# Performance work log

Hardware: AMD Instinct MI355X
Metric: run time of the kernel (lower is better)

The kernel has to match this reference:

```python
import jax, jax.numpy as jnp
import numpy as np

EPS = 1e-6

def _rms_norm(t, g):
    # t: [B, S, C] (applied before the view to heads, matching the torch code)
    y = t.astype(jnp.float32)
    y = jax.lax.rsqrt(jnp.mean(y * y, axis=-1, keepdims=True) + EPS)
    return (t * y * g).astype(t.dtype)

def _apply_rope(t, cos, sin):
    # t: [B, S, N, D]; cos/sin: [1, S, 1, D//2]; interleaved pair rotation
    b, s, n, d = t.shape
    tr = t.reshape(b, s, n, d // 2, 2)
    tre, tim = tr[..., 0], tr[..., 1]
    out = jnp.stack([tre * cos - tim * sin, tre * sin + tim * cos], axis=-1)
    return out.reshape(b, s, n, d)

def setup_inputs() -> dict:
    key = jax.random.key(0)
    ks = jax.random.split(key, 8)
    B, S, DIM, N, D = 2, 1024, 3072, 24, 128
    x = jax.random.normal(ks[0], (B, S, DIM), dtype=jnp.float32)
    seq_lens = jax.random.randint(ks[1], (B,), S // 2, S + 1, dtype=jnp.int32)
    grid_sizes = jnp.tile(jnp.array([[16, 8, 8]], dtype=jnp.int32), (B, 1))
    # rope angle table [1024, D//2]: pos * inv_freq
    inv_freq = 1.0 / (10000.0 ** (jnp.arange(D // 2, dtype=jnp.float32) * 2.0 / D))
    freqs = jnp.arange(1024, dtype=jnp.float32)[:, None] * inv_freq[None, :]
    sc = 1.0 / np.sqrt(DIM)
    Wq = jax.random.normal(ks[2], (DIM, DIM), dtype=jnp.float32) * sc
    Wk = jax.random.normal(ks[3], (DIM, DIM), dtype=jnp.float32) * sc
    Wv = jax.random.normal(ks[4], (DIM, DIM), dtype=jnp.float32) * sc
    Wo = jax.random.normal(ks[5], (DIM, DIM), dtype=jnp.float32) * sc
    bq = jnp.zeros((DIM,), jnp.float32); bk = jnp.zeros((DIM,), jnp.float32)
    bv = jnp.zeros((DIM,), jnp.float32); bo = jnp.zeros((DIM,), jnp.float32)
    gq = jnp.ones((DIM,), jnp.float32); gk = jnp.ones((DIM,), jnp.float32)
    return {"x": x, "seq_lens": seq_lens, "grid_sizes": grid_sizes, "freqs": freqs,
            "Wq": Wq, "bq": bq, "Wk": Wk, "bk": bk, "Wv": Wv, "bv": bv,
            "Wo": Wo, "bo": bo, "gq": gq, "gk": gk}

def reference(x, seq_lens, grid_sizes, freqs, Wq, bq, Wk, bk, Wv, bv, Wo, bo, gq, gk):
    b, s, dim = x.shape
    d = 2 * freqs.shape[1]          # head_dim
    n = dim // d                    # num_heads
    q = _rms_norm(x @ Wq.T + bq, gq).reshape(b, s, n, d)
    k = _rms_norm(x @ Wk.T + bk, gk).reshape(b, s, n, d)
    v = (x @ Wv.T + bv).reshape(b, s, n, d)
    ang = freqs[:s]                 # [S, D//2]
    cos = jnp.cos(ang)[None, :, None, :]
    sin = jnp.sin(ang)[None, :, None, :]
    q = _apply_rope(q, cos, sin)
    k = _apply_rope(k, cos, sin)
    # full attention (window_size = (-1,-1)), varlen key masking via seq_lens
    scale = d ** -0.5
    scores = jnp.einsum('bind,bjnd->bnij', q, k) * scale   # [B,N,S,S]
    key_valid = jnp.arange(s)[None, :] < seq_lens[:, None]  # [B,S]
    scores = jnp.where(key_valid[:, None, None, :], scores, jnp.finfo(scores.dtype).min)
    p = jax.nn.softmax(scores, axis=-1)
    out = jnp.einsum('bnij,bjnd->bind', p, v).reshape(b, s, dim)
    return out @ Wo.T + bo
```

## Files before the change

### kernel.cpp

```cpp
#include <hip/hip_runtime.h>
#include <cmath>

#define BB   2
#define SS   1024
#define DIMM 3072
#define NHH  24
#define HDD  128
#define MM   (BB * SS)

typedef _Float16 f16;
typedef __attribute__((ext_vector_type(8))) _Float16 half8;
typedef __attribute__((ext_vector_type(4))) float floatx4;
typedef unsigned int u32;
typedef const __attribute__((address_space(1))) u32* gp1;
typedef __attribute__((address_space(3))) u32* lp3;

__device__ __forceinline__ void gload_lds16(const void* g, void* l) {
    __builtin_amdgcn_global_load_lds((gp1)g, (lp3)l, 16, 0, 0);
}

__global__ __launch_bounds__(256) void cvt_f16_kernel(
    const float* __restrict__ in, f16* __restrict__ outp, int n8)
{
    int i = blockIdx.x * 256 + threadIdx.x;
    if (i >= n8) return;
    const float4* p = (const float4*)(in + (size_t)i * 8);
    float4 a = p[0], b = p[1];
    half8 h = {(f16)a.x, (f16)a.y, (f16)a.z, (f16)a.w,
               (f16)b.x, (f16)b.y, (f16)b.z, (f16)b.w};
    *(half8*)(outp + (size_t)i * 8) = h;
}

__global__ __launch_bounds__(256) void cvt3_f16_kernel(
    const float* __restrict__ w0, const float* __restrict__ w1,
    const float* __restrict__ w2, f16* __restrict__ outp, int n8each)
{
    int i = blockIdx.x * 256 + threadIdx.x;
    int sel = i / n8each;
    int j = i - sel * n8each;
    const float* in = sel == 0 ? w0 : (sel == 1 ? w1 : w2);
    const float4* p = (const float4*)(in + (size_t)j * 8);
    float4 a = p[0], b = p[1];
    half8 h = {(f16)a.x, (f16)a.y, (f16)a.z, (f16)a.w,
               (f16)b.x, (f16)b.y, (f16)b.z, (f16)b.w};
    *(half8*)(outp + (size_t)i * 8) = h;
}

__global__ __launch_bounds__(256) void cvt4_f16_kernel(
    const float* __restrict__ w0, const float* __restrict__ w1,
    const float* __restrict__ w2, const float* __restrict__ w3,
    f16* __restrict__ outp, int n8each)
{
    int i = blockIdx.x * 256 + threadIdx.x;
    int sel = i / n8each;
    int j = i - sel * n8each;
    const float* in = sel == 0 ? w0 : (sel == 1 ? w1 : (sel == 2 ? w2 : w3));
    const float4* p = (const float4*)(in + (size_t)j * 8);
    float4 a = p[0], b = p[1];
    half8 h = {(f16)a.x, (f16)a.y, (f16)a.z, (f16)a.w,
               (f16)b.x, (f16)b.y, (f16)b.z, (f16)b.w};
    *(half8*)(outp + (size_t)i * 8) = h;
}

template<bool QKV>
__global__ __launch_bounds__(256) void gemm_p32d4(
    const f16* __restrict__ A,
    const f16* __restrict__ W0, const f16* __restrict__ W1, const f16* __restrict__ W2,
    const float* __restrict__ b0, const float* __restrict__ b1, const float* __restrict__ b2,
    f16* __restrict__ D0, f16* __restrict__ D1, f16* __restrict__ D2,
    float* __restrict__ F)
{
    constexpr int K = DIMM;
    constexpr int NSTEP = K / 32;
    constexpr int TS = 128 * 32;
    __shared__ __align__(16) f16 As[5][TS];
    __shared__ __align__(16) f16 Bs[5][TS];

    const int tid  = threadIdx.x;
    const int lane = tid & 63;
    const int wave = tid >> 6;
    const int wm = wave >> 1, wn = wave & 1;
    const int lr = lane & 15;
    const int lq = lane >> 4;

    const int id  = blockIdx.x;
    const int cpx = (int)gridDim.x >> 3;
    const int swz = (id & 7) * cpx + (id >> 3);
    const int bm = (swz & 15) << 7;
    const int bn = (swz >> 4) << 7;

    const f16* Wh; const float* bias; f16* D = nullptr;
    int nloc = bn;
    if constexpr (QKV) {
        int sel = bn / DIMM;
        nloc = bn - sel * DIMM;
        Wh   = sel == 0 ? W0 : (sel == 1 ? W1 : W2);
        bias = sel == 0 ? b0 : (sel == 1 ? b1 : b2);
        D    = sel == 0 ? D0 : (sel == 1 ? D1 : D2);
    } else { Wh = W0; bias = b0; }

    const int r0 = tid >> 2;
    const int g0 = ((tid & 3) ^ ((r0 >> 1) & 3)) << 3;
    const int r1 = (tid + 256) >> 2;
    const int g1 = ((tid & 3) ^ ((r1 >> 1) & 3)) << 3;
    const f16* a0  = A  + (size_t)(bm   + r0) * K + g0;
    const f16* a1  = A  + (size_t)(bm   + r1) * K + g1;
    const f16* w0p = Wh + (size_t)(nloc + r0) * K + g0;
    const f16* w1p = Wh + (size_t)(nloc + r1) * K + g1;

    auto STAGE = [&](int t, int buf) {
        const int k0 = t * 32;
        gload_lds16(a0  + k0, &As[buf][(size_t)tid * 8]);
        gload_lds16(a1  + k0, &As[buf][(size_t)(tid + 256) * 8]);
        gload_lds16(w0p + k0, &Bs[buf][(size_t)tid * 8]);
        gload_lds16(w1p + k0, &Bs[buf][(size_t)(tid + 256) * 8]);
    };

    floatx4 acc[4][4];
#pragma unroll
    for (int i = 0; i < 4; ++i)
#pragma unroll
        for (int j = 0; j < 4; ++j) acc[i][j] = (floatx4){0.f, 0.f, 0.f, 0.f};

    auto COMPUTE = [&](int buf) {
        const f16* Ab = &As[buf][0];
        const f16* Bb = &Bs[buf][0];
        half8 af[4], bf[4];
#pragma unroll
        for (int i = 0; i < 4; ++i) {
            int ra = wm * 64 + i * 16 + lr;
            int rb = wn * 64 + i * 16 + lr;
            af[i] = *(const half8*)&Ab[ra * 32 + ((lq ^ ((ra >> 1) & 3)) << 3)];
            bf[i] = *(const half8*)&Bb[rb * 32 + ((lq ^ ((rb >> 1) & 3)) << 3)];
        }
#pragma unroll
        for (int mi = 0; mi < 4; ++mi)
#pragma unroll
            for (int ni = 0; ni < 4; ++ni)
                acc[mi][ni] = __builtin_amdgcn_mfma_f32_16x16x32_f16(af[mi], bf[ni], acc[mi][ni], 0, 0, 0);
    };

    STAGE(0, 0); STAGE(1, 1); STAGE(2, 2); STAGE(3, 3);
    asm volatile("s_waitcnt vmcnt(12)" ::: "memory");
    __builtin_amdgcn_s_barrier();

    int cur = 0, stg = 4;
    for (int ks = 0; ks < NSTEP; ++ks) {
        if (ks + 4 < NSTEP) STAGE(ks + 4, stg);
        COMPUTE(cur);
        const int rem = NSTEP - ks;
        if (rem > 4)       asm volatile("s_waitcnt vmcnt(12)" ::: "memory");
        else if (rem == 4) asm volatile("s_waitcnt vmcnt(8)"  ::: "memory");
        else if (rem == 3) asm volatile("s_waitcnt vmcnt(4)"  ::: "memory");
        else if (rem == 2) asm volatile("s_waitcnt vmcnt(0)"  ::: "memory");
        if (rem > 1) __builtin_amdgcn_s_barrier();
        cur = (cur == 4) ? 0 : cur + 1;
        stg = (stg == 4) ? 0 : stg + 1;
    }

    const int crow0 = bm + wm * 64 + (lq << 2);
    const int ccol0 = nloc + wn * 64;
#pragma unroll
    for (int ni = 0; ni < 4; ++ni) {
        const int col = ccol0 + ni * 16 + lr;
        const float bv = bias[col];
#pragma unroll
        for (int mi = 0; mi < 4; ++mi) {
            const int row = crow0 + mi * 16;
#pragma unroll
            for (int r2 = 0; r2 < 4; ++r2) {
                if constexpr (QKV)
                    D[(size_t)(row + r2) * DIMM + col] = (f16)(acc[mi][ni][r2] + bv);
                else
                    F[(size_t)(row + r2) * DIMM + col] = acc[mi][ni][r2] + bv;
            }
        }
    }
}

template<bool QKV>
__global__ __launch_bounds__(256) void gemm_p32(
    const f16* __restrict__ A,
    const f16* __restrict__ W0, const f16* __restrict__ W1, const f16* __restrict__ W2,
    const float* __restrict__ b0, const float* __restrict__ b1, const float* __restrict__ b2,
    f16* __restrict__ D0, f16* __restrict__ D1, f16* __restrict__ D2,
    float* __restrict__ F)
{
    constexpr int K = DIMM;
    constexpr int NSTEP = K / 32;
    constexpr int TS = 128 * 32;
    __shared__ __align__(16) f16 As[3][TS];
    __shared__ __align__(16) f16 Bs[3][TS];

    const int tid  = threadIdx.x;
    const int lane = tid & 63;
    const int wave = tid >> 6;
    const int wm = wave >> 1, wn = wave & 1;
    const int lr = lane & 15;
    const int lq = lane >> 4;

    const int id  = blockIdx.x;
    const int cpx = (int)gridDim.x >> 3;
    const int swz = (id & 7) * cpx + (id >> 3);
    const int bm = (swz & 15) << 7;
    const int bn = (swz >> 4) << 7;

    const f16* Wh; const float* bias; f16* D = nullptr;
    int nloc = bn;
    if constexpr (QKV) {
        int sel = bn / DIMM;
        nloc = bn - sel * DIMM;
        Wh   = sel == 0 ? W0 : (sel == 1 ? W1 : W2);
        bias = sel == 0 ? b0 : (sel == 1 ? b1 : b2);
        D    = sel == 0 ? D0 : (sel == 1 ? D1 : D2);
    } else { Wh = W0; bias = b0; }

    const int r0 = tid >> 2;
    const int g0 = ((tid & 3) ^ ((r0 >> 1) & 3)) << 3;
    const int r1 = (tid + 256) >> 2;
    const int g1 = ((tid & 3) ^ ((r1 >> 1) & 3)) << 3;
    const f16* a0  = A  + (size_t)(bm   + r0) * K + g0;
    const f16* a1  = A  + (size_t)(bm   + r1) * K + g1;
    const f16* w0p = Wh + (size_t)(nloc + r0) * K + g0;
    const f16* w1p = Wh + (size_t)(nloc + r1) * K + g1;

    auto STAGE = [&](int t, int buf) {
        const int k0 = t * 32;
        gload_lds16(a0  + k0, &As[buf][(size_t)tid * 8]);
        gload_lds16(a1  + k0, &As[buf][(size_t)(tid + 256) * 8]);
        gload_lds16(w0p + k0, &Bs[buf][(size_t)tid * 8]);
        gload_lds16(w1p + k0, &Bs[buf][(size_t)(tid + 256) * 8]);
    };

    floatx4 acc[4][4];
#pragma unroll
    for (int i = 0; i < 4; ++i)
#pragma unroll
        for (int j = 0; j < 4; ++j) acc[i][j] = (floatx4){0.f, 0.f, 0.f, 0.f};

    auto COMPUTE = [&](int buf) {
        const f16* Ab = &As[buf][0];
        const f16* Bb = &Bs[buf][0];
        half8 af[4], bf[4];
#pragma unroll
        for (int i = 0; i < 4; ++i) {
            int ra = wm * 64 + i * 16 + lr;
            int rb = wn * 64 + i * 16 + lr;
            af[i] = *(const half8*)&Ab[ra * 32 + ((lq ^ ((ra >> 1) & 3)) << 3)];
            bf[i] = *(const half8*)&Bb[rb * 32 + ((lq ^ ((rb >> 1) & 3)) << 3)];
        }
#pragma unroll
        for (int mi = 0; mi < 4; ++mi)
#pragma unroll
            for (int ni = 0; ni < 4; ++ni)
                acc[mi][ni] = __builtin_amdgcn_mfma_f32_16x16x32_f16(af[mi], bf[ni], acc[mi][ni], 0, 0, 0);
    };

    STAGE(0, 0);
    STAGE(1, 1);
    asm volatile("s_waitcnt vmcnt(4)" ::: "memory");
    __builtin_amdgcn_s_barrier();

    int cur = 0, stg = 2;
    for (int ks = 0; ks < NSTEP; ++ks) {
        const bool more = (ks + 2 < NSTEP);
        if (more) STAGE(ks + 2, stg);
        COMPUTE(cur);
        if (more) asm volatile("s_waitcnt vmcnt(4)" ::: "memory");
        else      asm volatile("s_waitcnt vmcnt(0)" ::: "memory");
        __builtin_amdgcn_s_barrier();
        cur = (cur == 2) ? 0 : cur + 1;
        stg = (stg == 2) ? 0 : stg + 1;
    }

    const int crow0 = bm + wm * 64 + (lq << 2);
    const int ccol0 = nloc + wn * 64;
#pragma unroll
    for (int ni = 0; ni < 4; ++ni) {
        const int col = ccol0 + ni * 16 + lr;
        const float bv = bias[col];
#pragma unroll
        for (int mi = 0; mi < 4; ++mi) {
            const int row = crow0 + mi * 16;
#pragma unroll
            for (int r2 = 0; r2 < 4; ++r2) {
                if constexpr (QKV)
                    D[(size_t)(row + r2) * DIMM + col] = (f16)(acc[mi][ni][r2] + bv);
                else
                    F[(size_t)(row + r2) * DIMM + col] = acc[mi][ni][r2] + bv;
            }
        }
    }
}

template<bool QKV>
__global__ __launch_bounds__(256) void gemm_f16m(
    const f16* __restrict__ A,
    const float* __restrict__ W0, const float* __restrict__ W1, const float* __restrict__ W2,
    const float* __restrict__ b0, const float* __restrict__ b1, const float* __restrict__ b2,
    f16* __restrict__ D0, f16* __restrict__ D1, f16* __restrict__ D2,
    float* __restrict__ F)
{
    constexpr int K = DIMM;
    constexpr int NSTEP = K / 32;
    __shared__ f16 As[128 * 32];
    __shared__ f16 Bs[128 * 32];

    const int tid  = threadIdx.x;
    const int lane = tid & 63;
    const int wave = tid >> 6;
    const int wm = wave >> 1, wn = wave & 1;
    const int lr = lane & 15;
    const int lq = lane >> 4;

    const int id  = blockIdx.x;
    const int cpx = (int)gridDim.x >> 3;
    const int swz = (id & 7) * cpx + (id >> 3);
    const int bm = (swz & 15) << 7;
    const int bn = (swz >> 4) << 7;

    const float* W; const float* bias; f16* D = nullptr;
    int nloc = bn;
    if constexpr (QKV) {
        int sel = bn / DIMM;
        nloc = bn - sel * DIMM;
        W    = sel == 0 ? W0 : (sel == 1 ? W1 : W2);
        bias = sel == 0 ? b0 : (sel == 1 ? b1 : b2);
        D    = sel == 0 ? D0 : (sel == 1 ? D1 : D2);
    } else { W = W0; bias = b0; }

    const int r0 = tid >> 2;
    const int c8 = (tid & 3) << 3;
    const float* bp0 = W + (size_t)(nloc + r0) * K + c8;
    const float* bp1 = W + (size_t)(nloc + r0 + 64) * K + c8;

    const int arow_l = lane >> 2;
    const int acol_l = (lane & 3) << 3;
    const f16* agbase = A + (size_t)bm * K;

    float4 sb00, sb01, sb10, sb11;
    auto LOADB = [&](int k0) {
        sb00 = *(const float4*)(bp0 + k0); sb01 = *(const float4*)(bp0 + k0 + 4);
        sb10 = *(const float4*)(bp1 + k0); sb11 = *(const float4*)(bp1 + k0 + 4);
    };
    auto STOREB = [&]() {
        half8 h0 = {(f16)sb00.x, (f16)sb00.y, (f16)sb00.z, (f16)sb00.w,
                    (f16)sb01.x, (f16)sb01.y, (f16)sb01.z, (f16)sb01.w};
        half8 h1 = {(f16)sb10.x, (f16)sb10.y, (f16)sb10.z, (f16)sb10.w,
                    (f16)sb11.x, (f16)sb11.y, (f16)sb11.z, (f16)sb11.w};
        *(half8*)&Bs[r0 * 32 + c8]        = h0;
        *(half8*)&Bs[(r0 + 64) * 32 + c8] = h1;
    };

    floatx4 acc[4][4];
#pragma unroll
    for (int i = 0; i < 4; ++i)
#pragma unroll
        for (int j = 0; j < 4; ++j) acc[i][j] = (floatx4){0.f, 0.f, 0.f, 0.f};

    LOADB(0);
    for (int ks = 0; ks < NSTEP; ++ks) {
        const int k0 = ks * 32;
        __syncthreads();
#pragma unroll
        for (int i = 0; i < 2; ++i) {
            int rbase = wave * 32 + i * 16;
            gload_lds16(agbase + (size_t)(rbase + arow_l) * K + k0 + acol_l,
                        &As[rbase * 32]);
        }
        STOREB();
        __syncthreads();
        if (ks + 1 < NSTEP) LOADB(k0 + 32);

        half8 af[4], bf[4];
#pragma unroll
        for (int i = 0; i < 4; ++i) {
            af[i] = *(const half8*)&As[(wm * 64 + i * 16 + lr) * 32 + lq * 8];
            bf[i] = *(const half8*)&Bs[(wn * 64 + i * 16 + lr) * 32 + lq * 8];
        }
#pragma unroll
        for (int mi = 0; mi < 4; ++mi)
#pragma unroll
            for (int ni = 0; ni < 4; ++ni)
                acc[mi][ni] = __builtin_amdgcn_mfma_f32_16x16x32_f16(af[mi], bf[ni], acc[mi][ni], 0, 0, 0);
    }

    const int crow0 = bm + wm * 64 + (lq << 2);
    const int ccol0 = nloc + wn * 64;
#pragma unroll
    for (int ni = 0; ni < 4; ++ni) {
        const int col = ccol0 + ni * 16 + lr;
        const float bv = bias[col];
#pragma unroll
        for (int mi = 0; mi < 4; ++mi) {
            const int row = crow0 + mi * 16;
#pragma unroll
            for (int r2 = 0; r2 < 4; ++r2) {
                if constexpr (QKV)
                    D[(size_t)(row + r2) * DIMM + col] = (f16)(acc[mi][ni][r2] + bv);
                else
                    F[(size_t)(row + r2) * DIMM + col] = acc[mi][ni][r2] + bv;
            }
        }
    }
}

__global__ __launch_bounds__(192) void rmsnorm_rope_f16(
    f16* __restrict__ q, f16* __restrict__ k,
    const float* __restrict__ gq, const float* __restrict__ gk,
    const float* __restrict__ freqs)
{
    f16* t = (blockIdx.y == 0) ? q : k;
    const float* g = (blockIdx.y == 0) ? gq : gk;
    const int row = blockIdx.x;
    const int s = row & (SS - 1);
    const int tid = threadIdx.x;
    f16* base = t + (size_t)row * DIMM + tid * 16;

    half8 v0 = *(const half8*)base;
    half8 v1 = *(const half8*)(base + 8);
    float v[16];
#pragma unroll
    for (int j = 0; j < 8; ++j) { v[j] = (float)v0[j]; v[8 + j] = (float)v1[j]; }

    float ssq = 0.f;
#pragma unroll
    for (int j = 0; j < 16; ++j) ssq += v[j] * v[j];
#pragma unroll
    for (int off = 32; off > 0; off >>= 1) ssq += __shfl_down(ssq, off, 64);
    __shared__ float red[3];
    if ((tid & 63) == 0) red[tid >> 6] = ssq;
    __syncthreads();
    float tot = red[0] + red[1] + red[2];
    float sc = rsqrtf(tot * (1.0f / (float)DIMM) + 1e-6f);

    const float* gp = g + tid * 16;
    float y[16];
#pragma unroll
    for (int j = 0; j < 16; ++j) y[j] = v[j] * sc * gp[j];

#pragma unroll
    for (int p = 0; p < 8; ++p) {
        int idx = tid * 16 + 2 * p;
        int f = (idx & 127) >> 1;
        float ang = freqs[s * 64 + f];
        float cc = cosf(ang), sn = sinf(ang);
        float e = y[2 * p], o = y[2 * p + 1];
        y[2 * p]     = e * cc - o * sn;
        y[2 * p + 1] = e * sn + o * cc;
    }
    half8 o0, o1;
#pragma unroll
    for (int j = 0; j < 8; ++j) { o0[j] = (f16)y[j]; o1[j] = (f16)y[8 + j]; }
    *(half8*)base       = o0;
    *(half8*)(base + 8) = o1;
}

__global__ __launch_bounds__(256) void flash_attn_f16(
    const f16* __restrict__ Q, const f16* __restrict__ K,
    const f16* __restrict__ V, const int* __restrict__ seq_lens,
    f16* __restrict__ O)
{
    __shared__ __align__(16) f16 QPs[64 * 128];
    __shared__ __align__(16) f16 Ks[64 * 128];
    __shared__ __align__(16) f16 Vt[128 * 64];

    const int tid  = threadIdx.x;
    const int lane = tid & 63;
    const int wave = tid >> 6;
    const int ln = lane & 15;
    const int lq = lane >> 4;
    const int i0 = blockIdx.x * 64;
    const int h  = blockIdx.y;
    const int b  = blockIdx.z;
    const int slen = seq_lens[b];
    const float scale = 0.08838834764831845f;
    const size_t gstride = NHH * HDD;

    const f16* Qg = Q + ((size_t)(b * SS + i0) * NHH + h) * HDD;
#pragma unroll
    for (int rep = 0; rep < 4; ++rep) {
        int u = tid + rep * 256;
        int r = u >> 4, d0 = (u & 15) << 3;
        half8 qv = *(const half8*)(Qg + (size_t)r * gstride + d0);
        *(half8*)(QPs + r * 128 + (d0 ^ ((r & 7) << 3))) = qv;
    }
    __syncthreads();

    half8 qfrag[4];
    {
        int rq = wave * 16 + ln;
#pragma unroll
        for (int ks = 0; ks < 4; ++ks)
            qfrag[ks] = *(const half8*)(QPs + rq * 128 + ((ks * 32 + lq * 8) ^ ((rq & 7) << 3)));
    }

    floatx4 accO[8];
#pragma unroll
    for (int dt = 0; dt < 8; ++dt) accO[dt] = (floatx4){0.f, 0.f, 0.f, 0.f};
    float mrow[4] = {-3.0e38f, -3.0e38f, -3.0e38f, -3.0e38f};
    float lrow[4] = {0.f, 0.f, 0.f, 0.f};

    const int nT = (slen + 63) >> 6;
    for (int t = 0; t < nT; ++t) {
        const int j0g = t * 64;
        __syncthreads();

        const f16* Kg = K + ((size_t)(b * SS + j0g) * NHH + h) * HDD;
#pragma unroll
        for (int rep = 0; rep < 4; ++rep) {
            int u = tid + rep * 256;
            int r = u >> 4, d0 = (u & 15) << 3;
            half8 kv = *(const half8*)(Kg + (size_t)r * gstride + d0);
            *(half8*)(Ks + r * 128 + (d0 ^ ((r & 7) << 3))) = kv;
        }
        const f16* Vg = V + ((size_t)(b * SS + j0g) * NHH + h) * HDD;
#pragma unroll
        for (int rep = 0; rep < 2; ++rep) {
            int u = tid + rep * 256;
            int jp = u & 31, j0 = jp * 2;
            int d0 = (u >> 5) << 3;
            half8 va = *(const half8*)(Vg + (size_t)j0 * gstride + d0);
            half8 vb = *(const half8*)(Vg + (size_t)(j0 + 1) * gstride + d0);
#pragma unroll
            for (int i = 0; i < 8; ++i) {
                int d = d0 + i;
                union { f16 h[2]; u32 w; } pk;
                pk.h[0] = va[i]; pk.h[1] = vb[i];
                *(u32*)(Vt + d * 64 + (j0 ^ ((d & 7) << 3))) = pk.w;
            }
        }
        __syncthreads();

        floatx4 acc_s[4];
#pragma unroll
        for (int nt = 0; nt < 4; ++nt) {
            acc_s[nt] = (floatx4){0.f, 0.f, 0.f, 0.f};
            int rk = nt * 16 + ln;
#pragma unroll
            for (int ks = 0; ks < 4; ++ks) {
                half8 kf = *(const half8*)(Ks + rk * 128 + ((ks * 32 + lq * 8) ^ ((rk & 7) << 3)));
                acc_s[nt] = __builtin_amdgcn_mfma_f32_16x16x32_f16(qfrag[ks], kf, acc_s[nt], 0, 0, 0);
            }
        }

        float s[4][4];
#pragma unroll
        for (int nt = 0; nt < 4; ++nt) {
            int j = j0g + nt * 16 + ln;
            bool valid = (j < slen);
#pragma unroll
            for (int r = 0; r < 4; ++r)
                s[nt][r] = valid ? acc_s[nt][r] * scale : -3.0e38f;
        }
        float fct[4];
#pragma unroll
        for (int r = 0; r < 4; ++r) {
            float m4 = fmaxf(fmaxf(s[0][r], s[1][r]), fmaxf(s[2][r], s[3][r]));
            m4 = fmaxf(m4, __shfl_xor(m4, 1, 64));
            m4 = fmaxf(m4, __shfl_xor(m4, 2, 64));
            m4 = fmaxf(m4, __shfl_xor(m4, 4, 64));
            m4 = fmaxf(m4, __shfl_xor(m4, 8, 64));
            float mn = fmaxf(mrow[r], m4);
            fct[r] = __expf(mrow[r] - mn);
            mrow[r] = mn;
            float ls = 0.f;
#pragma unroll
            for (int nt = 0; nt < 4; ++nt) {
                float p = __expf(s[nt][r] - mn);
                s[nt][r] = p;
                ls += p;
            }
            ls += __shfl_xor(ls, 1, 64);
            ls += __shfl_xor(ls, 2, 64);
            ls += __shfl_xor(ls, 4, 64);
            ls += __shfl_xor(ls, 8, 64);
            lrow[r] = lrow[r] * fct[r] + ls;
        }

#pragma unroll
        for (int nt = 0; nt < 4; ++nt) {
#pragma unroll
            for (int r = 0; r < 4; ++r) {
                int rw = lq * 4 + r;
                int j = nt * 16 + ln;
                QPs[(wave * 16 + rw) * 128 + (j ^ ((rw & 7) << 3))] = (f16)s[nt][r];
            }
        }

#pragma unroll
        for (int dt = 0; dt < 8; ++dt)
#pragma unroll
            for (int r = 0; r < 4; ++r) accO[dt][r] *= fct[r];

        half8 pfrag[2];
#pragma unroll
        for (int js = 0; js < 2; ++js)
            pfrag[js] = *(const half8*)(QPs + (wave * 16 + ln) * 128 + ((js * 32 + lq * 8) ^ ((ln & 7) << 3)));
#pragma unroll
        for (int dt = 0; dt < 8; ++dt) {
            int d = dt * 16 + ln;
#pragma unroll
            for (int js = 0; js < 2; ++js) {
                half8 vf = *(const half8*)(Vt + d * 64 + ((js * 32 + lq * 8) ^ ((d & 7) << 3)));
                accO[dt] = __builtin_amdgcn_mfma_f32_16x16x32_f16(pfrag[js], vf, accO[dt], 0, 0, 0);
            }
        }
    }

    float linv[4];
#pragma unroll
    for (int r = 0; r < 4; ++r) linv[r] = 1.0f / lrow[r];
    f16* Og = O + ((size_t)(b * SS + i0) * NHH + h) * HDD;
#pragma unroll
    for (int dt = 0; dt < 8; ++dt) {
#pragma unroll
        for (int r = 0; r < 4; ++r) {
            int qr = wave * 16 + lq * 4 + r;
            int d = dt * 16 + ln;
            Og[(size_t)qr * gstride + d] = (f16)(accO[dt][r] * linv[r]);
        }
    }
}

extern "C" void kernel_launch(void* const* d_in, const int* in_sizes, int n_in,
                              void* d_out, int out_size, void* d_ws, size_t ws_size,
                              hipStream_t stream)
{
    const float* x     = (const float*)d_in[0];
    const int*   seq   = (const int*)d_in[1];
    const float* freqs = (const float*)d_in[3];
    const float* Wq    = (const float*)d_in[4];
    const float* bq    = (const float*)d_in[5];
    const float* Wk    = (const float*)d_in[6];
    const float* bk    = (const float*)d_in[7];
    const float* Wv    = (const float*)d_in[8];
    const float* bv    = (const float*)d_in[9];
    const float* Wo    = (const float*)d_in[10];
    const float* bo    = (const float*)d_in[11];
    const float* gq    = (const float*)d_in[12];
    const float* gk    = (const float*)d_in[13];

    float* out = (float*)d_out;
    const size_t MD = (size_t)MM * DIMM;
    const size_t WD = (size_t)DIMM * DIMM;

    f16* X16 = (f16*)d_ws;
    f16* q16 = X16 + MD;
    f16* k16 = X16 + 2 * MD;
    f16* v16 = (f16*)d_out;

    const int nMD8 = (int)(MD / 8);
    const int nWD8 = (int)(WD / 8);
    const size_t need1 = (3 * MD + 3 * WD) * sizeof(f16);
    const size_t need2 = (3 * MD + 4 * WD) * sizeof(f16);

    cvt_f16_kernel<<<nMD8 / 256, 256, 0, stream>>>(x, X16, nMD8);

    if (ws_size >= need1) {
        f16* Wq16 = X16 + 3 * MD;
        f16* Wk16 = Wq16 + WD;
        f16* Wv16 = Wk16 + WD;
        f16* Wo16;
        if (ws_size >= need2) {
            Wo16 = Wv16 + WD;
            cvt4_f16_kernel<<<4 * nWD8 / 256, 256, 0, stream>>>(Wq, Wk, Wv, Wo, Wq16, nWD8);
        } else {
            Wo16 = Wq16;
            cvt3_f16_kernel<<<3 * nWD8 / 256, 256, 0, stream>>>(Wq, Wk, Wv, Wq16, nWD8);
        }
        gemm_p32d4<true><<<(MM / 128) * (3 * DIMM / 128), 256, 0, stream>>>(
            X16, Wq16, Wk16, Wv16, bq, bk, bv, q16, k16, v16, nullptr);
        if (ws_size < need2)
            cvt_f16_kernel<<<nWD8 / 256, 256, 0, stream>>>(Wo, Wo16, nWD8);
        rmsnorm_rope_f16<<<dim3(MM, 2), 192, 0, stream>>>(q16, k16, gq, gk, freqs);
        flash_attn_f16<<<dim3(SS / 64, NHH, BB), 256, 0, stream>>>(q16, k16, v16, seq, X16);
        gemm_p32<false><<<(MM / 128) * (DIMM / 128), 256, 0, stream>>>(
            X16, Wo16, nullptr, nullptr, bo, nullptr, nullptr, nullptr, nullptr, nullptr, out);
    } else {
        gemm_f16m<true><<<(MM / 128) * (3 * DIMM / 128), 256, 0, stream>>>(
            X16, Wq, Wk, Wv, bq, bk, bv, q16, k16, v16, nullptr);
        rmsnorm_rope_f16<<<dim3(MM, 2), 192, 0, stream>>>(q16, k16, gq, gk, freqs);
        flash_attn_f16<<<dim3(SS / 64, NHH, BB), 256, 0, stream>>>(q16, k16, v16, seq, X16);
        gemm_f16m<false><<<(MM / 128) * (DIMM / 128), 256, 0, stream>>>(
            X16, Wo, nullptr, nullptr, bo, nullptr, nullptr, nullptr, nullptr, nullptr, out);
    }
}
```

Baseline: 401.7 us.

## Enlarge QKV GEMM tile to 256x128 with 8 waves and triple buffering

The fused QKV projection GEMM now uses 512-thread blocks computing 256x128 output tiles, with the four row-wave groups sharing one B tile. This halves the B-operand traffic per FLOP and halves the grid size. The LDS pipeline drops from 5 buffers with prefetch depth 4 to 3 buffers with depth 2, which lowers shared memory per block. In exchange, less global-load latency is hidden, and the larger blocks with fewer of them may reduce occupancy and load balance across CUs.

Result: faster. 386.0 us (-3.9%).

```diff
diff --git a/kernel.cpp b/kernel.cpp
--- a/kernel.cpp
+++ b/kernel.cpp
@@ -63,7 +63,7 @@
 }
 
 template<bool QKV>
-__global__ __launch_bounds__(256) void gemm_p32d4(
+__global__ __launch_bounds__(512) void gemm_w256(
     const f16* __restrict__ A,
     const f16* __restrict__ W0, const f16* __restrict__ W1, const f16* __restrict__ W2,
     const float* __restrict__ b0, const float* __restrict__ b1, const float* __restrict__ b2,
@@ -72,9 +72,10 @@
 {
     constexpr int K = DIMM;
     constexpr int NSTEP = K / 32;
-    constexpr int TS = 128 * 32;
-    __shared__ __align__(16) f16 As[5][TS];
-    __shared__ __align__(16) f16 Bs[5][TS];
+    constexpr int ATS = 256 * 32;
+    constexpr int BTS = 128 * 32;
+    __shared__ __align__(16) f16 As[3][ATS];
+    __shared__ __align__(16) f16 Bs[3][BTS];
 
     const int tid  = threadIdx.x;
     const int lane = tid & 63;
@@ -86,8 +87,8 @@
     const int id  = blockIdx.x;
     const int cpx = (int)gridDim.x >> 3;
     const int swz = (id & 7) * cpx + (id >> 3);
-    const int bm = (swz & 15) << 7;
-    const int bn = (swz >> 4) << 7;
+    const int bm = (swz & 7) << 8;
+    const int bn = (swz >> 3) << 7;
 
     const f16* Wh; const float* bias; f16* D = nullptr;
     int nloc = bn;
@@ -99,21 +100,19 @@
         D    = sel == 0 ? D0 : (sel == 1 ? D1 : D2);
     } else { Wh = W0; bias = b0; }
 
-    const int r0 = tid >> 2;
-    const int g0 = ((tid & 3) ^ ((r0 >> 1) & 3)) << 3;
-    const int r1 = (tid + 256) >> 2;
-    const int g1 = ((tid & 3) ^ ((r1 >> 1) & 3)) << 3;
-    const f16* a0  = A  + (size_t)(bm   + r0) * K + g0;
-    const f16* a1  = A  + (size_t)(bm   + r1) * K + g1;
-    const f16* w0p = Wh + (size_t)(nloc + r0) * K + g0;
-    const f16* w1p = Wh + (size_t)(nloc + r1) * K + g1;
+    const int ra0 = tid >> 2;
+    const int ga0 = ((tid & 3) ^ ((ra0 >> 1) & 3)) << 3;
+    const int ra1 = (tid + 512) >> 2;
+    const int ga1 = ((tid & 3) ^ ((ra1 >> 1) & 3)) << 3;
+    const f16* a0  = A  + (size_t)(bm   + ra0) * K + ga0;
+    const f16* a1  = A  + (size_t)(bm   + ra1) * K + ga1;
+    const f16* w0p = Wh + (size_t)(nloc + ra0) * K + ga0;
 
     auto STAGE = [&](int t, int buf) {
         const int k0 = t * 32;
         gload_lds16(a0  + k0, &As[buf][(size_t)tid * 8]);
-        gload_lds16(a1  + k0, &As[buf][(size_t)(tid + 256) * 8]);
+        gload_lds16(a1  + k0, &As[buf][(size_t)(tid + 512) * 8]);
         gload_lds16(w0p + k0, &Bs[buf][(size_t)tid * 8]);
-        gload_lds16(w1p + k0, &Bs[buf][(size_t)(tid + 256) * 8]);
     };
 
     floatx4 acc[4][4];
@@ -140,22 +139,21 @@
                 acc[mi][ni] = __builtin_amdgcn_mfma_f32_16x16x32_f16(af[mi], bf[ni], acc[mi][ni], 0, 0, 0);
     };
 
-    STAGE(0, 0); STAGE(1, 1); STAGE(2, 2); STAGE(3, 3);
-    asm volatile("s_waitcnt vmcnt(12)" ::: "memory");
+    STAGE(0, 0);
+    STAGE(1, 1);
+    asm volatile("s_waitcnt vmcnt(3)" ::: "memory");
     __builtin_amdgcn_s_barrier();
 
-    int cur = 0, stg = 4;
+    int cur = 0, stg = 2;
     for (int ks = 0; ks < NSTEP; ++ks) {
-        if (ks + 4 < NSTEP) STAGE(ks + 4, stg);
+        const bool more = (ks + 2 < NSTEP);
+        if (more) STAGE(ks + 2, stg);
         COMPUTE(cur);
-        const int rem = NSTEP - ks;
-        if (rem > 4)       asm volatile("s_waitcnt vmcnt(12)" ::: "memory");
-        else if (rem == 4) asm volatile("s_waitcnt vmcnt(8)"  ::: "memory");
-        else if (rem == 3) asm volatile("s_waitcnt vmcnt(4)"  ::: "memory");
-        else if (rem == 2) asm volatile("s_waitcnt vmcnt(0)"  ::: "memory");
-        if (rem > 1) __builtin_amdgcn_s_barrier();
-        cur = (cur == 4) ? 0 : cur + 1;
-        stg = (stg == 4) ? 0 : stg + 1;
+        if (more) asm volatile("s_waitcnt vmcnt(3)" ::: "memory");
+        else      asm volatile("s_waitcnt vmcnt(0)" ::: "memory");
+        __builtin_amdgcn_s_barrier();
+        cur = (cur == 2) ? 0 : cur + 1;
+        stg = (stg == 2) ? 0 : stg + 1;
     }
 
     const int crow0 = bm + wm * 64 + (lq << 2);
@@ -669,7 +667,7 @@
             Wo16 = Wq16;
             cvt3_f16_kernel<<<3 * nWD8 / 256, 256, 0, stream>>>(Wq, Wk, Wv, Wq16, nWD8);
         }
-        gemm_p32d4<true><<<(MM / 128) * (3 * DIMM / 128), 256, 0, stream>>>(
+        gemm_w256<true><<<(MM / 256) * (3 * DIMM / 128), 512, 0, stream>>>(
             X16, Wq16, Wk16, Wv16, bq, bk, bv, q16, k16, v16, nullptr);
         if (ws_size < need2)
             cvt_f16_kernel<<<nWD8 / 256, 256, 0, stream>>>(Wo, Wo16, nWD8);
```
